# Optimization experiments

Measured on AMD Instinct MI355X. Metric: run time of the kernel, lower is better.

## Reference

```python
import jax, jax.numpy as jnp
import numpy as np

B, T, D, H, K = 8, 512, 768, 8, 4
HD = D // H
SCALE = 1.0 / float(np.sqrt(HD))
EPS = 1e-5


def _ln(x, g, b):
    m = jnp.mean(x, -1, keepdims=True)
    v = jnp.mean((x - m) ** 2, -1, keepdims=True)
    return (x - m) * jax.lax.rsqrt(v + EPS) * g + b


def _attn(q, k, v, mask=None):
    # q,k,v: [B,T,D] -> multi-head scaled dot product, returns [B,T,D]
    sp = lambda t: t.reshape(B, T, H, HD).transpose(0, 2, 1, 3)  # [B,H,T,hd]
    a = jnp.einsum('bhqd,bhkd->bhqk', sp(q), sp(k)) * SCALE
    if mask is not None:
        a = jnp.where(mask, -jnp.inf, a)
    a = jax.nn.softmax(a, -1)
    o = jnp.einsum('bhqk,bhkd->bhqd', a, sp(v))
    return o.transpose(0, 2, 1, 3).reshape(B, T, D)


def setup_inputs() -> dict:
    key = jax.random.key(0)
    ks = iter(jax.random.split(key, 20))
    n = lambda shp: jax.random.normal(next(ks), shp, jnp.float32) * 0.02
    z = lambda shp: jnp.zeros(shp, jnp.float32)
    o = lambda shp: jnp.ones(shp, jnp.float32)
    return dict(
        x=jax.random.normal(next(ks), (B, T, D), jnp.float32),
        router_w1=n((128, D)), router_b1=z((128,)),
        router_w2=n((2 * K, 128)), router_b2=z((2 * K,)),
        norm_s_g=o((D,)), norm_s_b=z((D,)),
        norm_t_g=o((D,)), norm_t_b=z((D,)),
        norm_mlp_g=o((D,)), norm_mlp_b=z((D,)),
        sp_wqkv=n((K, 3 * D, D)), sp_bqkv=z((K, 3 * D)),
        sp_wo=n((K, D, D)), sp_bo=z((K, D)),
        tp_wq=n((K, D, D)), tp_bq=z((K, D)),
        tp_wk=n((K, D, D)), tp_bk=z((K, D)),
        tp_wv=n((K, D, D)), tp_bv=z((K, D)),
        tp_wo=n((K, D, D)), tp_bo=z((K, D)),
        cross_wqkv=n((3 * D, D)), cross_bqkv=z((3 * D,)),
        cross_wo=n((D, D)), cross_bo=z((D,)),
        mlp_w1=n((4 * D, D)), mlp_b1=z((4 * D,)),
        mlp_w2=n((D, 4 * D)), mlp_b2=z((D,)),
    )


def _forward(x, router_w1, router_b1, router_w2, router_b2,
             norm_s_g, norm_s_b, norm_t_g, norm_t_b, norm_mlp_g, norm_mlp_b,
             sp_wqkv, sp_bqkv, sp_wo, sp_bo,
             tp_wq, tp_bq, tp_wk, tp_bk, tp_wv, tp_bv, tp_wo, tp_bo,
             cross_wqkv, cross_bqkv, cross_wo, cross_bo,
             mlp_w1, mlp_b1, mlp_w2, mlp_b2):
    # --- router: top-1 expert per sample for each branch ---
    h = jax.nn.gelu(x.mean(1) @ router_w1.T + router_b1, approximate=False)
    route = jax.nn.softmax(h @ router_w2.T + router_b2, -1)  # [B, 2K]
    idx_s = jnp.argmax(route[:, :K], -1)  # [B] top-1 spatial expert
    idx_t = jnp.argmax(route[:, K:], -1)  # [B] top-1 temporal expert

    # --- spatial branch: per-sample routed MultiheadAttention (self-attn) ---
    xn = _ln(x, norm_s_g, norm_s_b)
    qkv = jnp.einsum('btd,bed->bte', xn, sp_wqkv[idx_s]) + sp_bqkv[idx_s][:, None, :]
    q, k, v = jnp.split(qkv, 3, -1)
    so = _attn(q, k, v)
    spatial_out = jnp.einsum('btd,bed->bte', so, sp_wo[idx_s]) + sp_bo[idx_s][:, None, :]

    # --- temporal branch: per-sample routed causal attention (with residual) ---
    xt = _ln(x, norm_t_g, norm_t_b)
    qt = jnp.einsum('btd,bed->bte', xt, tp_wq[idx_t]) + tp_bq[idx_t][:, None, :]
    kt = jnp.einsum('btd,bed->bte', xt, tp_wk[idx_t]) + tp_bk[idx_t][:, None, :]
    vt = jnp.einsum('btd,bed->bte', xt, tp_wv[idx_t]) + tp_bv[idx_t][:, None, :]
    causal = jnp.triu(jnp.ones((T, T), bool), 1)
    to = _attn(qt, kt, vt, mask=causal)
    to = jnp.einsum('btd,bed->bte', to, tp_wo[idx_t]) + tp_bo[idx_t][:, None, :]
    temporal_out = xt + to  # CausalTimeAttention2 adds residual to its (normed) query

    # --- cross attention fusing the two branches ---
    cq = spatial_out @ cross_wqkv[:D].T + cross_bqkv[:D]
    ck = temporal_out @ cross_wqkv[D:2 * D].T + cross_bqkv[D:2 * D]
    cv = temporal_out @ cross_wqkv[2 * D:].T + cross_bqkv[2 * D:]
    fused = _attn(cq, ck, cv) @ cross_wo.T + cross_bo

    x = x + fused
    y = jax.nn.gelu(_ln(x, norm_mlp_g, norm_mlp_b) @ mlp_w1.T + mlp_b1, approximate=False)
    x = x + (y @ mlp_w2.T + mlp_b2)
    return x


def reference(x, router_w1, router_b1, router_w2, router_b2,
              norm_s_g, norm_s_b, norm_t_g, norm_t_b, norm_mlp_g, norm_mlp_b,
              sp_wqkv, sp_bqkv, sp_wo, sp_bo,
              tp_wq, tp_bq, tp_wk, tp_bk, tp_wv, tp_bv, tp_wo, tp_bo,
              cross_wqkv, cross_bqkv, cross_wo, cross_bo,
              mlp_w1, mlp_b1, mlp_w2, mlp_b2):
    return _forward(x, router_w1, router_b1, router_w2, router_b2,
                    norm_s_g, norm_s_b, norm_t_g, norm_t_b, norm_mlp_g, norm_mlp_b,
                    sp_wqkv, sp_bqkv, sp_wo, sp_bo,
                    tp_wq, tp_bq, tp_wk, tp_bk, tp_wv, tp_bv, tp_wo, tp_bo,
                    cross_wqkv, cross_bqkv, cross_wo, cross_bo,
                    mlp_w1, mlp_b1, mlp_w2, mlp_b2)
```

## Files before the change

kernel.cpp:

```cpp
#include <hip/hip_runtime.h>
#include <math.h>

#define BB 8
#define TT 512
#define DD 768
#define HH 8
#define HDIM 96
#define DDDD 589824LL

typedef short s16x8 __attribute__((ext_vector_type(8)));
typedef float f32x4 __attribute__((ext_vector_type(4)));
typedef unsigned short u16;

__device__ inline unsigned short f2bf(float f) {
    union { float f; unsigned u; } v; v.f = f;
    unsigned u = v.u;
    unsigned r = (u + 0x7fffu + ((u >> 16) & 1u)) >> 16;
    return (unsigned short)r;
}

__device__ inline float bf2f(u16 h) {
    union { unsigned u; float f; } v; v.u = ((unsigned)h) << 16; return v.f;
}

__device__ inline float gelu_exact(float x) {
    return 0.5f * x * (1.0f + erff(x * 0.70710678118654752440f));
}

__device__ __forceinline__ void gload16(const void* g, void* l) {
    __builtin_amdgcn_global_load_lds(
        (const __attribute__((address_space(1))) unsigned int*)g,
        (__attribute__((address_space(3))) unsigned int*)l,
        16, 0, 0);
}

__device__ __forceinline__ long long tix(int m, int k, int ldn) {
    return ((long long)(m >> 6) * (ldn >> 3) + (k >> 3)) * 512 + ((m & 63) << 3) + (k & 7);
}

#define CUM1  7077888LL
#define CUM2  9437184LL
#define CUM3  11796480LL
#define CUM4  14155776LL
#define CUM5  16515072LL
#define CUM6  18874368LL
#define CUM7  20643840LL
#define CUM8  21233664LL
#define CUM9  23592960LL
#define CUM10 25952256LL

__global__ __launch_bounds__(256) void cvt_kernel(
    const float* __restrict__ s0, const float* __restrict__ s1,
    const float* __restrict__ s2, const float* __restrict__ s3,
    const float* __restrict__ s4, const float* __restrict__ s5,
    const float* __restrict__ s6, const float* __restrict__ s7,
    const float* __restrict__ s8, const float* __restrict__ s9,
    u16* __restrict__ dpool)
{
    long long g = ((long long)blockIdx.x * 256 + threadIdx.x) * 8;
    if (g >= CUM10) return;
    const float* s; long long i, base; int n, k, K = 768;
    const long long SZQKV = 2304LL * 768;
    if (g < CUM1) {
        s = s0; i = g;
        long long e = i / SZQKV, r = i - e * SZQKV;
        n = (int)(r / 768); k = (int)(r % 768); base = e * 3 * DDDD;
    } else if (g < CUM2) {
        s = s1; i = g - CUM1;
        long long e = i / DDDD, r = i - e * DDDD;
        n = (int)(r / 768); k = (int)(r % 768); base = CUM1 + e * DDDD;
    } else if (g < CUM5) {
        int tp = (g < CUM3) ? 0 : (g < CUM4) ? 1 : 2;
        s = (tp == 0) ? s2 : (tp == 1) ? s3 : s4;
        i = g - ((tp == 0) ? CUM2 : (tp == 1) ? CUM3 : CUM4);
        long long e = i / DDDD, r = i - e * DDDD;
        n = tp * 768 + (int)(r / 768); k = (int)(r % 768);
        base = CUM2 + e * 3 * DDDD;
    } else if (g < CUM6) {
        s = s5; i = g - CUM5;
        long long e = i / DDDD, r = i - e * DDDD;
        n = (int)(r / 768); k = (int)(r % 768); base = CUM5 + e * DDDD;
    } else if (g < CUM7) {
        s = s6; i = g - CUM6;
        n = (int)(i / 768); k = (int)(i % 768); base = CUM6;
    } else if (g < CUM8) {
        s = s7; i = g - CUM7;
        n = (int)(i / 768); k = (int)(i % 768); base = CUM7;
    } else if (g < CUM9) {
        s = s8; i = g - CUM8;
        n = (int)(i / 768); k = (int)(i % 768); base = CUM8;
    } else {
        s = s9; i = g - CUM9;
        n = (int)(i / 3072); k = (int)(i % 3072); base = CUM9; K = 3072;
    }
    float4 a = *(const float4*)(s + i);
    float4 b = *(const float4*)(s + i + 4);
    s16x8 o;
    o[0] = f2bf(a.x); o[1] = f2bf(a.y); o[2] = f2bf(a.z); o[3] = f2bf(a.w);
    o[4] = f2bf(b.x); o[5] = f2bf(b.y); o[6] = f2bf(b.z); o[7] = f2bf(b.w);
    long long d = base + (((long long)(n >> 7) * (K >> 3) + (k >> 3)) << 10) + ((n & 127) << 3);
    *(s16x8*)(dpool + d) = o;
}

__global__ __launch_bounds__(256) void pack_tpb_kernel(
    const float* __restrict__ bq, const float* __restrict__ bk,
    const float* __restrict__ bv, float* __restrict__ dst)
{
    int t = blockIdx.x * 256 + threadIdx.x;
    if (t >= 4 * 2304) return;
    int e = t / 2304, n = t - e * 2304;
    float v = (n < 768) ? bq[e * 768 + n]
            : (n < 1536) ? bk[e * 768 + n - 768]
            : bv[e * 768 + n - 1536];
    dst[t] = v;
}

#define SLABA 2048
#define SLABB 4096

template<int OUT_MODE, int RES_MODE>
__global__ __launch_bounds__(256) void gemm_bf16_kernel(
    const u16* __restrict__ A, long long sAb,
    const u16* __restrict__ B, const int* __restrict__ bidx, long long sBexp,
    void* __restrict__ Cv, long long sCb, int ldc,
    const float* __restrict__ bias, long long sBiasExp,
    const void* __restrict__ residv, long long sResB, int ldr,
    int act, int N, int K)
{
    int nbx = gridDim.x, nby = gridDim.y;
    int nblk = nbx * nby * (int)gridDim.z;
    int lin = blockIdx.x + nbx * (blockIdx.y + nby * blockIdx.z);
    int q = nblk >> 3, r = nblk & 7;
    int xcd = lin & 7, pos = lin >> 3;
    int nl = (xcd < r ? xcd * (q + 1) : r * (q + 1) + (xcd - r) * q) + pos;
    int bx = nl % nbx; int t1 = nl / nbx; int by = t1 % nby; int bz = t1 / nby;

    int zb = bz;
    int kw8 = K >> 3;
    const u16* Ab = A + zb * sAb + (long long)by * kw8 * 512;
    const u16* Bb = B + (bidx ? (long long)bidx[zb] * sBexp : 0)
                      + (long long)bx * kw8 * 1024;
    const float* biasb = bias ? (bias + (bidx ? (long long)bidx[zb] * sBiasExp : 0)) : nullptr;

    __shared__ __align__(16) u16 As[6][SLABA];
    __shared__ __align__(16) u16 Bs[6][SLABB];

    int tid = threadIdx.x;
    int wave = tid >> 6, lane = tid & 63;
    int wr = wave >> 1, wc = wave & 1;
    int lrow = lane & 15, lkg = lane >> 4;

    f32x4 acc[2][4];
    #pragma unroll
    for (int i = 0; i < 2; i++)
        #pragma unroll
        for (int j = 0; j < 4; j++)
            acc[i][j] = (f32x4){0.f, 0.f, 0.f, 0.f};

    const u16* agt = Ab + tid * 8;
    const u16* bgt = Bb + tid * 8;
    u16* al  = (u16*)As + tid * 8;
    u16* bl0 = (u16*)Bs + tid * 8;
    u16* bl1 = (u16*)Bs + (tid + 256) * 8;

    auto stage = [&](int slab, int buf) {
        gload16(agt + slab * SLABA,        al  + buf * SLABA);
        gload16(bgt + slab * SLABB,        bl0 + buf * SLABB);
        gload16(bgt + slab * SLABB + 2048, bl1 + buf * SLABB);
    };

    int nK = K >> 5;
    stage(0, 0); stage(1, 1); stage(2, 2); stage(3, 3); stage(4, 4);

    int cur = 0, nxt = 5;
    for (int kt = 0; kt < nK; ++kt) {
        int infl = nK - 1 - kt; if (infl > 4) infl = 4;
        switch (infl) {
            case 4: asm volatile("s_waitcnt vmcnt(12)" ::: "memory"); break;
            case 3: asm volatile("s_waitcnt vmcnt(9)" ::: "memory"); break;
            case 2: asm volatile("s_waitcnt vmcnt(6)" ::: "memory"); break;
            case 1: asm volatile("s_waitcnt vmcnt(3)" ::: "memory"); break;
            default: asm volatile("s_waitcnt vmcnt(0)" ::: "memory"); break;
        }
        __builtin_amdgcn_s_barrier();
        __builtin_amdgcn_sched_barrier(0);
        if (kt + 5 < nK) stage(kt + 5, nxt);

        const u16* Asb = &As[cur][0];
        const u16* Bsb = &Bs[cur][0];
        s16x8 af[2], bf[4];
        #pragma unroll
        for (int i = 0; i < 2; ++i)
            af[i] = *(const s16x8*)&Asb[((lkg) * 64 + wr * 32 + i * 16 + lrow) * 8];
        #pragma unroll
        for (int j = 0; j < 4; ++j)
            bf[j] = *(const s16x8*)&Bsb[((lkg) * 128 + wc * 64 + j * 16 + lrow) * 8];
        #pragma unroll
        for (int i = 0; i < 2; ++i)
            #pragma unroll
            for (int j = 0; j < 4; ++j)
                acc[i][j] = __builtin_amdgcn_mfma_f32_16x16x32_bf16(af[i], bf[j], acc[i][j], 0, 0, 0);
        cur = (cur + 1 == 6) ? 0 : cur + 1;
        nxt = (nxt + 1 == 6) ? 0 : nxt + 1;
    }

    int n0 = bx * 128;
    int m0 = by * 64;
    float* Cf = (float*)Cv + zb * sCb;
    u16* Ch = (u16*)Cv + zb * sCb;
    const float* Rf = (const float*)residv + zb * sResB;
    const u16* Rh = (const u16*)residv + zb * sResB;
    int col16 = lane & 15;
    int rq = (lane >> 4) * 4;
    #pragma unroll
    for (int j = 0; j < 4; ++j) {
        int n = n0 + wc * 64 + j * 16 + col16;
        float bv = biasb ? biasb[n] : 0.0f;
        #pragma unroll
        for (int i = 0; i < 2; ++i) {
            #pragma unroll
            for (int r2 = 0; r2 < 4; ++r2) {
                int m = m0 + wr * 32 + i * 16 + rq + r2;
                float v = acc[i][j][r2] + bv;
                if (act == 1) v = gelu_exact(v);
                if (RES_MODE == 1) v += Rf[(long long)m * ldr + n];
                if (RES_MODE == 2) v += bf2f(Rh[tix(m, n, ldr)]);
                if (OUT_MODE == 0) Cf[(long long)m * ldc + n] = v;
                if (OUT_MODE == 1) Ch[(long long)m * ldc + n] = f2bf(v);
                if (OUT_MODE == 2) Ch[tix(m, n, ldc)] = f2bf(v);
            }
        }
    }
}

__global__ __launch_bounds__(256, 2) void attn_kernel(
    const u16* __restrict__ QKV, u16* __restrict__ Out,
    int causal, float scale)
{
    int qt = blockIdx.x;
    int bh = blockIdx.y;
    int b = bh >> 3;
    int h = bh & 7;
    const u16* Qb = QKV + (long long)b * TT * 3 * DD + (long long)h * HDIM;
    const u16* Kb = Qb + DD;
    const u16* Vb = Qb + 2 * DD;
    u16* Ob = Out + (long long)b * TT * DD;

    __shared__ __align__(16) u16 Qs[64 * 104];
    __shared__ __align__(16) u16 Ks[64 * 104];
    __shared__ __align__(16) u16 Vs[96 * 72];
    __shared__ __align__(16) u16 Ps[64 * 72];

    int tid = threadIdx.x;
    int wave = tid >> 6;
    int lane = tid & 63;
    int col16 = lane & 15;
    int lkg = lane >> 4;
    int lk = lkg * 8;
    int m0 = qt * 64;

    #pragma unroll
    for (int it = 0; it < 3; ++it) {
        int s = tid + it * 256;
        int r = s / 12, c8 = (s % 12) * 8;
        *(s16x8*)&Qs[r * 104 + c8] = *(const s16x8*)(Qb + (long long)(m0 + r) * (3 * DD) + c8);
    }
    __syncthreads();

    s16x8 qf[3];
    #pragma unroll
    for (int kk = 0; kk < 3; ++kk)
        qf[kk] = *(const s16x8*)&Qs[(wave * 16 + col16) * 104 + kk * 32 + lk];

    f32x4 acc[32];
    #pragma unroll
    for (int n = 0; n < 32; ++n) acc[n] = (f32x4){0.f, 0.f, 0.f, 0.f};

    #pragma unroll
    for (int kt = 0; kt < 8; ++kt) {
        #pragma unroll
        for (int it = 0; it < 3; ++it) {
            int s = tid + it * 256;
            int r = s / 12, c8 = (s % 12) * 8;
            *(s16x8*)&Ks[r * 104 + c8] = *(const s16x8*)(Kb + (long long)(kt * 64 + r) * (3 * DD) + c8);
        }
        __syncthreads();
        #pragma unroll
        for (int kk = 0; kk < 3; ++kk) {
            #pragma unroll
            for (int j = 0; j < 4; ++j) {
                s16x8 bfr = *(const s16x8*)&Ks[(j * 16 + col16) * 104 + kk * 32 + lk];
                acc[kt * 4 + j] = __builtin_amdgcn_mfma_f32_16x16x32_bf16(qf[kk], bfr, acc[kt * 4 + j], 0, 0, 0);
            }
        }
        __syncthreads();
    }

    int rowbase = m0 + wave * 16 + lkg * 4;
    float mx[4];
    #pragma unroll
    for (int r = 0; r < 4; ++r) mx[r] = -3.0e38f;
    #pragma unroll
    for (int n = 0; n < 32; ++n) {
        int colg = n * 16 + col16;
        #pragma unroll
        for (int r = 0; r < 4; ++r) {
            float v = acc[n][r] * scale;
            if (causal && colg > rowbase + r) v = -3.0e38f;
            acc[n][r] = v;
            mx[r] = fmaxf(mx[r], v);
        }
    }
    #pragma unroll
    for (int m = 1; m <= 8; m <<= 1)
        #pragma unroll
        for (int r = 0; r < 4; ++r)
            mx[r] = fmaxf(mx[r], __shfl_xor(mx[r], m, 64));

    float sum[4] = {0.f, 0.f, 0.f, 0.f};
    #pragma unroll
    for (int n = 0; n < 32; ++n) {
        #pragma unroll
        for (int r = 0; r < 4; ++r) {
            float e = __expf(acc[n][r] - mx[r]);
            acc[n][r] = e;
            sum[r] += e;
        }
    }
    #pragma unroll
    for (int m = 1; m <= 8; m <<= 1)
        #pragma unroll
        for (int r = 0; r < 4; ++r)
            sum[r] += __shfl_xor(sum[r], m, 64);
    float inv[4];
    #pragma unroll
    for (int r = 0; r < 4; ++r) inv[r] = 1.0f / sum[r];

    f32x4 oacc[6];
    #pragma unroll
    for (int j = 0; j < 6; ++j) oacc[j] = (f32x4){0.f, 0.f, 0.f, 0.f};

    #pragma unroll
    for (int kt = 0; kt < 8; ++kt) {
        __syncthreads();
        #pragma unroll
        for (int j = 0; j < 4; ++j) {
            #pragma unroll
            for (int r = 0; r < 4; ++r)
                Ps[(wave * 16 + lkg * 4 + r) * 72 + j * 16 + col16] = f2bf(acc[kt * 4 + j][r]);
        }
        #pragma unroll
        for (int it = 0; it < 3; ++it) {
            int s = tid + it * 256;
            int key = s / 12, c8 = (s % 12) * 8;
            s16x8 v = *(const s16x8*)(Vb + (long long)(kt * 64 + key) * (3 * DD) + c8);
            #pragma unroll
            for (int e = 0; e < 8; ++e)
                Vs[(c8 + e) * 72 + key] = (u16)v[e];
        }
        __syncthreads();
        #pragma unroll
        for (int kk = 0; kk < 2; ++kk) {
            s16x8 pf = *(const s16x8*)&Ps[(wave * 16 + col16) * 72 + kk * 32 + lk];
            #pragma unroll
            for (int j = 0; j < 6; ++j) {
                s16x8 vf = *(const s16x8*)&Vs[(j * 16 + col16) * 72 + kk * 32 + lk];
                oacc[j] = __builtin_amdgcn_mfma_f32_16x16x32_bf16(pf, vf, oacc[j], 0, 0, 0);
            }
        }
    }

    int rquad = lkg * 4;
    #pragma unroll
    for (int j = 0; j < 6; ++j) {
        int d = h * 96 + j * 16 + col16;
        #pragma unroll
        for (int r = 0; r < 4; ++r) {
            int row = m0 + wave * 16 + rquad + r;
            Ob[tix(row, d, DD)] = f2bf(oacc[j][r] * inv[r]);
        }
    }
}

__global__ __launch_bounds__(256) void ln_kernel(
    const float* __restrict__ x, const float* __restrict__ g,
    const float* __restrict__ b, u16* __restrict__ out)
{
    long long row = blockIdx.x;
    const float* xr = x + row * DD;
    u16* ob = out + (row >> 9) * ((long long)TT * DD);
    int m = (int)(row & 511);
    int t = threadIdx.x;
    float vals[3];
    float s = 0.f, ss = 0.f;
    #pragma unroll
    for (int i = 0; i < 3; i++) {
        float v = xr[t + i * 256];
        vals[i] = v; s += v; ss += v * v;
    }
    __shared__ float rs[256], rss[256];
    rs[t] = s; rss[t] = ss; __syncthreads();
    for (int k = 128; k > 0; k >>= 1) {
        if (t < k) { rs[t] += rs[t + k]; rss[t] += rss[t + k]; }
        __syncthreads();
    }
    float mean = rs[0] * (1.0f / DD);
    float var = rss[0] * (1.0f / DD) - mean * mean;
    float inv = rsqrtf(var + 1e-5f);
    #pragma unroll
    for (int i = 0; i < 3; i++) {
        int d = t + i * 256;
        ob[tix(m, d, DD)] = f2bf((vals[i] - mean) * inv * g[d] + b[d]);
    }
}

__global__ __launch_bounds__(256) void mean_part_kernel(
    const float* __restrict__ x, float* __restrict__ part)
{
    int b = blockIdx.x, dseg = blockIdx.y, rc = blockIdx.z;
    int d = dseg * 256 + threadIdx.x;
    const float* xb = x + (long long)b * TT * DD;
    float s = 0.f;
    int r0 = rc * 64;
    for (int r = r0; r < r0 + 64; ++r) s += xb[(long long)r * DD + d];
    part[((long long)b * 8 + rc) * DD + d] = s;
}

__global__ __launch_bounds__(128) void router_kernel(
    const float* __restrict__ part, const float* __restrict__ w1,
    const float* __restrict__ b1, const float* __restrict__ w2,
    const float* __restrict__ b2, int* __restrict__ idx)
{
    int b = blockIdx.x, t = threadIdx.x;
    __shared__ float xm[DD];
    __shared__ float h[128];
    __shared__ float logits[8];
    for (int i = t; i < DD; i += 128) {
        float s = 0.f;
        for (int rc = 0; rc < 8; ++rc) s += part[((long long)b * 8 + rc) * DD + i];
        xm[i] = s * (1.0f / TT);
    }
    __syncthreads();
    {
        float s = b1[t];
        const float* w = w1 + (long long)t * DD;
        for (int d = 0; d < DD; ++d) s += xm[d] * w[d];
        h[t] = gelu_exact(s);
    }
    __syncthreads();
    if (t < 8) {
        float s = b2[t];
        const float* w = w2 + t * 128;
        for (int d = 0; d < 128; ++d) s += h[d] * w[d];
        logits[t] = s;
    }
    __syncthreads();
    if (t == 0) {
        int bsix = 0;
        for (int i = 1; i < 4; i++) if (logits[i] > logits[bsix]) bsix = i;
        int btix = 4;
        for (int i = 5; i < 8; i++) if (logits[i] > logits[btix]) btix = i;
        idx[b] = bsix;
        idx[b + BB] = btix - 4;
    }
}

static void run_gemm2(hipStream_t stream,
    const u16* A, long long sAb,
    const u16* B, const int* bidx, long long sBexp,
    void* C, long long sCb, int ldc,
    const float* bias, long long sBiasExp,
    const void* resid, long long sResB, int ldr,
    int act, int N, int K, int outmode, int resmode)
{
    dim3 grid(N / 128, 8, BB);
    if (outmode == 1)
        gemm_bf16_kernel<1, 0><<<grid, 256, 0, stream>>>(A, sAb, B, bidx, sBexp,
            C, sCb, ldc, bias, sBiasExp, resid, sResB, ldr, act, N, K);
    else if (outmode == 2 && resmode == 0)
        gemm_bf16_kernel<2, 0><<<grid, 256, 0, stream>>>(A, sAb, B, bidx, sBexp,
            C, sCb, ldc, bias, sBiasExp, resid, sResB, ldr, act, N, K);
    else if (outmode == 2)
        gemm_bf16_kernel<2, 2><<<grid, 256, 0, stream>>>(A, sAb, B, bidx, sBexp,
            C, sCb, ldc, bias, sBiasExp, resid, sResB, ldr, act, N, K);
    else
        gemm_bf16_kernel<0, 1><<<grid, 256, 0, stream>>>(A, sAb, B, bidx, sBexp,
            C, sCb, ldc, bias, sBiasExp, resid, sResB, ldr, act, N, K);
}

extern "C" void kernel_launch(void* const* d_in, const int* in_sizes, int n_in,
                              void* d_out, int out_size, void* d_ws, size_t ws_size,
                              hipStream_t stream)
{
    const float* x       = (const float*)d_in[0];
    const float* rw1     = (const float*)d_in[1];
    const float* rb1     = (const float*)d_in[2];
    const float* rw2     = (const float*)d_in[3];
    const float* rb2     = (const float*)d_in[4];
    const float* gs      = (const float*)d_in[5];
    const float* bs      = (const float*)d_in[6];
    const float* gt      = (const float*)d_in[7];
    const float* btt     = (const float*)d_in[8];
    const float* gm      = (const float*)d_in[9];
    const float* bm      = (const float*)d_in[10];
    const float* sp_wqkv = (const float*)d_in[11];
    const float* sp_bqkv = (const float*)d_in[12];
    const float* sp_wo   = (const float*)d_in[13];
    const float* sp_bo   = (const float*)d_in[14];
    const float* tp_wq   = (const float*)d_in[15];
    const float* tp_bq   = (const float*)d_in[16];
    const float* tp_wk   = (const float*)d_in[17];
    const float* tp_bk   = (const float*)d_in[18];
    const float* tp_wv   = (const float*)d_in[19];
    const float* tp_bv   = (const float*)d_in[20];
    const float* tp_wo   = (const float*)d_in[21];
    const float* tp_bo   = (const float*)d_in[22];
    const float* c_wqkv  = (const float*)d_in[23];
    const float* c_bqkv  = (const float*)d_in[24];
    const float* c_wo    = (const float*)d_in[25];
    const float* c_bo    = (const float*)d_in[26];
    const float* m_w1    = (const float*)d_in[27];
    const float* m_b1    = (const float*)d_in[28];
    const float* m_w2    = (const float*)d_in[29];
    const float* m_b2    = (const float*)d_in[30];
    float* out = (float*)d_out;

    float* ws = (float*)d_ws;
    size_t o = 0;
    float* part  = ws + o; o += (size_t)BB * 8 * DD;
    int*   idx   = (int*)(ws + o); o += 16;
    float* tpb   = ws + o; o += 4 * 2304;
    float* x1b   = ws + o; o += (size_t)4096 * DD;
    u16* xnb   = (u16*)(ws + o); o += (size_t)4096 * DD / 2;
    u16* tmp1b = (u16*)(ws + o); o += (size_t)4096 * DD / 2;
    u16* tmp2b = (u16*)(ws + o); o += (size_t)4096 * DD / 2;
    u16* soutb = (u16*)(ws + o); o += (size_t)4096 * DD / 2;
    u16* toutb = (u16*)(ws + o); o += (size_t)4096 * DD / 2;
    u16* qkvb  = (u16*)(ws + o); o += (size_t)4096 * 2304 / 2;
    u16* yb    = (u16*)(ws + o); o += (size_t)4096 * 3072 / 2;
    u16* wpool = (u16*)(ws + o); o += (size_t)CUM10 / 2;

    u16* w_sp_qkv = wpool;
    u16* w_sp_wo  = wpool + CUM1;
    u16* w_tp_qkv = wpool + CUM2;
    u16* w_tp_o   = wpool + CUM5;
    u16* w_c_qkv  = wpool + CUM6;
    u16* w_c_wo   = wpool + CUM7;
    u16* w_m1     = wpool + CUM8;
    u16* w_m2     = wpool + CUM9;

    int* idx_s = idx;
    int* idx_t = idx + BB;

    const long long sTD  = (long long)TT * DD;
    const long long sT3D = (long long)TT * 3 * DD;
    const long long sT4D = (long long)TT * 4 * DD;
    const float qk_scale = 1.0f / sqrtf((float)HDIM);

    cvt_kernel<<<(int)((CUM10 / 8 + 255) / 256), 256, 0, stream>>>(
        sp_wqkv, sp_wo, tp_wq, tp_wk, tp_wv, tp_wo, c_wqkv, c_wo, m_w1, m_w2, wpool);
    pack_tpb_kernel<<<36, 256, 0, stream>>>(tp_bq, tp_bk, tp_bv, tpb);

    mean_part_kernel<<<dim3(BB, 3, 8), 256, 0, stream>>>(x, part);
    router_kernel<<<BB, 128, 0, stream>>>(part, rw1, rb1, rw2, rb2, idx);

    ln_kernel<<<4096, 256, 0, stream>>>(x, gs, bs, xnb);
    run_gemm2(stream, xnb, sTD, w_sp_qkv, idx_s, 3 * DDDD,
              qkvb, sT3D, 3 * DD, sp_bqkv, 3 * DD, nullptr, 0, 0,
              0, 3 * DD, DD, 1, 0);
    attn_kernel<<<dim3(TT / 64, BB * HH), 256, 0, stream>>>(qkvb, tmp1b, 0, qk_scale);
    run_gemm2(stream, tmp1b, sTD, w_sp_wo, idx_s, DDDD,
              soutb, sTD, DD, sp_bo, DD, nullptr, 0, 0,
              0, DD, DD, 2, 0);

    ln_kernel<<<4096, 256, 0, stream>>>(x, gt, btt, xnb);
    run_gemm2(stream, xnb, sTD, w_tp_qkv, idx_t, 3 * DDDD,
              qkvb, sT3D, 3 * DD, tpb, 3 * DD, nullptr, 0, 0,
              0, 3 * DD, DD, 1, 0);
    attn_kernel<<<dim3(TT / 64, BB * HH), 256, 0, stream>>>(qkvb, tmp1b, 1, qk_scale);
    run_gemm2(stream, tmp1b, sTD, w_tp_o, idx_t, DDDD,
              toutb, sTD, DD, tp_bo, DD, xnb, sTD, DD,
              0, DD, DD, 2, 2);

    run_gemm2(stream, soutb, sTD, w_c_qkv, nullptr, 0,
              qkvb, sT3D, 3 * DD, c_bqkv, 0, nullptr, 0, 0,
              0, DD, DD, 1, 0);
    run_gemm2(stream, toutb, sTD, w_c_qkv + DDDD, nullptr, 0,
              qkvb + DD, sT3D, 3 * DD, c_bqkv + DD, 0, nullptr, 0, 0,
              0, 2 * DD, DD, 1, 0);
    attn_kernel<<<dim3(TT / 64, BB * HH), 256, 0, stream>>>(qkvb, tmp1b, 0, qk_scale);
    run_gemm2(stream, tmp1b, sTD, w_c_wo, nullptr, 0,
              x1b, sTD, DD, c_bo, 0, x, sTD, DD,
              0, DD, DD, 0, 1);

    ln_kernel<<<4096, 256, 0, stream>>>(x1b, gm, bm, tmp2b);
    run_gemm2(stream, tmp2b, sTD, w_m1, nullptr, 0,
              yb, sT4D, 4 * DD, m_b1, 0, nullptr, 0, 0,
              1, 4 * DD, DD, 2, 0);
    run_gemm2(stream, yb, sT4D, w_m2, nullptr, 0,
              out, sTD, DD, m_b2, 0, x1b, sTD, DD,
              0, DD, 4 * DD, 0, 1);
}
```

Before: 738.5 us.

## Load GEMM A fragments directly to registers, drop A shared-memory staging

The A operand tile is no longer staged through LDS. Each lane loads its MFMA fragments straight from global memory into a three-deep register ring, while B keeps its six-slab LDS pipeline. The K loop is unrolled by six so slab indices are compile-time constants, and the vmcnt waits are simplified. This cuts LDS traffic and footprint, which may help occupancy, but it relies on nK being a multiple of six and on the global A reads being coalesced enough in the packed layout.

```diff
diff --git a/kernel.cpp b/kernel.cpp
--- a/kernel.cpp
+++ b/kernel.cpp
@@ -115,7 +115,6 @@
     dst[t] = v;
 }
 
-#define SLABA 2048
 #define SLABB 4096
 
 template<int OUT_MODE, int RES_MODE>
@@ -142,7 +141,6 @@
                       + (long long)bx * kw8 * 1024;
     const float* biasb = bias ? (bias + (bidx ? (long long)bidx[zb] * sBiasExp : 0)) : nullptr;
 
-    __shared__ __align__(16) u16 As[6][SLABA];
     __shared__ __align__(16) u16 Bs[6][SLABB];
 
     int tid = threadIdx.x;
@@ -157,51 +155,64 @@
         for (int j = 0; j < 4; j++)
             acc[i][j] = (f32x4){0.f, 0.f, 0.f, 0.f};
 
-    const u16* agt = Ab + tid * 8;
+    long long aoff0 = (long long)lkg * 512 + (wr * 32 + 0 * 16 + lrow) * 8;
+    long long aoff1 = (long long)lkg * 512 + (wr * 32 + 1 * 16 + lrow) * 8;
+
     const u16* bgt = Bb + tid * 8;
-    u16* al  = (u16*)As + tid * 8;
     u16* bl0 = (u16*)Bs + tid * 8;
     u16* bl1 = (u16*)Bs + (tid + 256) * 8;
 
-    auto stage = [&](int slab, int buf) {
-        gload16(agt + slab * SLABA,        al  + buf * SLABA);
-        gload16(bgt + slab * SLABB,        bl0 + buf * SLABB);
-        gload16(bgt + slab * SLABB + 2048, bl1 + buf * SLABB);
-    };
+    s16x8 abuf[3][2];
 
     int nK = K >> 5;
-    stage(0, 0); stage(1, 1); stage(2, 2); stage(3, 3); stage(4, 4);
-
-    int cur = 0, nxt = 5;
-    for (int kt = 0; kt < nK; ++kt) {
-        int infl = nK - 1 - kt; if (infl > 4) infl = 4;
-        switch (infl) {
-            case 4: asm volatile("s_waitcnt vmcnt(12)" ::: "memory"); break;
-            case 3: asm volatile("s_waitcnt vmcnt(9)" ::: "memory"); break;
-            case 2: asm volatile("s_waitcnt vmcnt(6)" ::: "memory"); break;
-            case 1: asm volatile("s_waitcnt vmcnt(3)" ::: "memory"); break;
-            default: asm volatile("s_waitcnt vmcnt(0)" ::: "memory"); break;
-        }
-        __builtin_amdgcn_s_barrier();
-        __builtin_amdgcn_sched_barrier(0);
-        if (kt + 5 < nK) stage(kt + 5, nxt);
-
-        const u16* Asb = &As[cur][0];
-        const u16* Bsb = &Bs[cur][0];
-        s16x8 af[2], bf[4];
-        #pragma unroll
-        for (int i = 0; i < 2; ++i)
-            af[i] = *(const s16x8*)&Asb[((lkg) * 64 + wr * 32 + i * 16 + lrow) * 8];
-        #pragma unroll
-        for (int j = 0; j < 4; ++j)
-            bf[j] = *(const s16x8*)&Bsb[((lkg) * 128 + wc * 64 + j * 16 + lrow) * 8];
-        #pragma unroll
-        for (int i = 0; i < 2; ++i)
+
+    gload16(bgt,            bl0);
+    gload16(bgt + 2048,     bl1);
+    gload16(bgt + SLABB,        bl0 + SLABB);
+    gload16(bgt + SLABB + 2048, bl1 + SLABB);
+    gload16(bgt + 2 * SLABB,        bl0 + 2 * SLABB);
+    gload16(bgt + 2 * SLABB + 2048, bl1 + 2 * SLABB);
+    abuf[0][0] = *(const s16x8*)(Ab + aoff0);
+    abuf[0][1] = *(const s16x8*)(Ab + aoff1);
+    gload16(bgt + 3 * SLABB,        bl0 + 3 * SLABB);
+    gload16(bgt + 3 * SLABB + 2048, bl1 + 3 * SLABB);
+    abuf[1][0] = *(const s16x8*)(Ab + 2048 + aoff0);
+    abuf[1][1] = *(const s16x8*)(Ab + 2048 + aoff1);
+    gload16(bgt + 4 * SLABB,        bl0 + 4 * SLABB);
+    gload16(bgt + 4 * SLABB + 2048, bl1 + 4 * SLABB);
+
+    for (int ktb = 0; ktb < nK; ktb += 6) {
+        #pragma unroll
+        for (int u = 0; u < 6; ++u) {
+            int kt = ktb + u;
+            if (kt + 6 <= nK) asm volatile("s_waitcnt vmcnt(6)" ::: "memory");
+            else              asm volatile("s_waitcnt vmcnt(0)" ::: "memory");
+            __builtin_amdgcn_s_barrier();
+            __builtin_amdgcn_sched_barrier(0);
+
+            if (kt + 2 < nK) {
+                const u16* ap = Ab + (long long)(kt + 2) * 2048;
+                abuf[(u + 2) % 3][0] = *(const s16x8*)(ap + aoff0);
+                abuf[(u + 2) % 3][1] = *(const s16x8*)(ap + aoff1);
+            }
+            if (kt + 5 < nK) {
+                const u16* bp = bgt + (long long)(kt + 5) * SLABB;
+                int sl = (u + 5) % 6;
+                gload16(bp,        bl0 + sl * SLABB);
+                gload16(bp + 2048, bl1 + sl * SLABB);
+            }
+
+            const u16* Bsb = &Bs[u][0];
+            s16x8 bf[4];
             #pragma unroll
             for (int j = 0; j < 4; ++j)
-                acc[i][j] = __builtin_amdgcn_mfma_f32_16x16x32_bf16(af[i], bf[j], acc[i][j], 0, 0, 0);
-        cur = (cur + 1 == 6) ? 0 : cur + 1;
-        nxt = (nxt + 1 == 6) ? 0 : nxt + 1;
+                bf[j] = *(const s16x8*)&Bsb[(lkg * 128 + wc * 64 + j * 16 + lrow) * 8];
+            #pragma unroll
+            for (int i = 0; i < 2; ++i)
+                #pragma unroll
+                for (int j = 0; j < 4; ++j)
+                    acc[i][j] = __builtin_amdgcn_mfma_f32_16x16x32_bf16(abuf[u % 3][i], bf[j], acc[i][j], 0, 0, 0);
+        }
     }
 
     int n0 = bx * 128;
```

Result: faster. 625.0 us (-15.4%).
